# Optimization experiments

Measured on AMD Instinct MI355X. Metric: run time of the kernel, lower is better.

Reference implementation:

```python
import jax, jax.numpy as jnp
import numpy as np

N = 100000
E = 1600000
DIN = 128
HID = 128
EPS = 1e-5


def setup_inputs() -> dict:
    key = jax.random.key(0)
    ks = jax.random.split(key, 16)
    s = lambda i, shape, sc=0.05: jax.random.normal(ks[i], shape, dtype=jnp.float32) * sc
    inp = {
        "x": jax.random.normal(ks[0], (N, DIN), dtype=jnp.float32),
        "edge_index": jax.random.randint(ks[1], (2, E), 0, N, dtype=jnp.int64),
        # layer 1
        "W1": s(2, (DIN, HID)), "b1": jnp.zeros((HID,), jnp.float32),
        "g1": jnp.ones((HID,), jnp.float32), "be1": jnp.zeros((HID,), jnp.float32),
        "m1": s(3, (HID,)), "v1": jax.random.uniform(ks[4], (HID,), jnp.float32) + 0.5,
        # layer 2
        "W2": s(5, (HID, HID)), "b2": jnp.zeros((HID,), jnp.float32),
        "g2": jnp.ones((HID,), jnp.float32), "be2": jnp.zeros((HID,), jnp.float32),
        "m2": s(6, (HID,)), "v2": jax.random.uniform(ks[7], (HID,), jnp.float32) + 0.5,
        # classifier
        "Wc1": s(8, (HID, HID // 2)), "bc1": jnp.zeros((HID // 2,), jnp.float32),
        "Wc2": s(9, (HID // 2, 2)), "bc2": jnp.zeros((2,), jnp.float32),
    }
    return inp


def _gnn_layer(x, W, b, src, dst):
    # linear then scatter-mean of source features onto destinations
    h = x @ W + b                                    # [N, HID]
    msg_sum = jax.ops.segment_sum(h[src], dst, num_segments=N)   # [N, HID]
    cnt = jax.ops.segment_sum(jnp.ones((src.shape[0],), h.dtype), dst, num_segments=N)
    return msg_sum / cnt[:, None]                    # self-loops guarantee cnt >= 1


def _bn(x, g, be, m, v):
    return (x - m) * jax.lax.rsqrt(v + EPS) * g + be


def reference(x, edge_index, W1, b1, g1, be1, m1, v1, W2, b2, g2, be2, m2, v2, Wc1, bc1, Wc2, bc2):
    # add self loops (PyG add_self_loops appends [i, i])
    loop = jnp.arange(N, dtype=edge_index.dtype)
    src = jnp.concatenate([edge_index[0], loop])
    dst = jnp.concatenate([edge_index[1], loop])

    h = _gnn_layer(x, W1, b1, src, dst)
    h = jax.nn.relu(_bn(h, g1, be1, m1, v1))
    h = _gnn_layer(h, W2, b2, src, dst)
    h = jax.nn.relu(_bn(h, g2, be2, m2, v2))

    h = jax.nn.relu(h @ Wc1 + bc1)
    return h @ Wc2 + bc2                              # logits [N, 2]
```

## Files before the change

### kernel.cpp

```cpp
#include <hip/hip_runtime.h>
#include <hip/hip_bf16.h>

#define EPS 1e-5f

__global__ __launch_bounds__(256) void k_zero(int* p, int n) {
    int i = blockIdx.x * 256 + threadIdx.x;
    if (i < n) p[i] = 0;
}

__global__ __launch_bounds__(256) void k_hist(const int* __restrict__ dst,
                                              int* __restrict__ counts, int nE) {
    int i = blockIdx.x * 256 + threadIdx.x;
    if (i < nE) atomicAdd(&counts[dst[i]], 1);
}

__global__ __launch_bounds__(256) void k_scan1(const int* __restrict__ counts,
                                               int* __restrict__ bsums, int n) {
    __shared__ int sdata[256];
    int base = blockIdx.x * 2048;
    int t = threadIdx.x;
    int s = 0;
#pragma unroll
    for (int i = 0; i < 8; ++i) {
        int idx = base + t * 8 + i;
        if (idx < n) s += counts[idx];
    }
    sdata[t] = s;
    __syncthreads();
    for (int off = 128; off > 0; off >>= 1) {
        if (t < off) sdata[t] += sdata[t + off];
        __syncthreads();
    }
    if (t == 0) bsums[blockIdx.x] = sdata[0];
}

__global__ __launch_bounds__(64) void k_scan2(int* __restrict__ bsums, int nb) {
    if (threadIdx.x == 0 && blockIdx.x == 0) {
        int acc = 0;
        for (int i = 0; i < nb; ++i) { int v = bsums[i]; bsums[i] = acc; acc += v; }
    }
}

__global__ __launch_bounds__(256) void k_scan3(const int* __restrict__ counts,
                                               const int* __restrict__ bsums,
                                               int* __restrict__ rowstart,
                                               int n, int nE) {
    __shared__ int sth[256];
    int base = blockIdx.x * 2048;
    int t = threadIdx.x;
    int loc[8];
    int s = 0;
#pragma unroll
    for (int i = 0; i < 8; ++i) {
        int idx = base + t * 8 + i;
        loc[i] = s;
        s += (idx < n) ? counts[idx] : 0;
    }
    sth[t] = s;
    __syncthreads();
    for (int off = 1; off < 256; off <<= 1) {
        int tmp = (t >= off) ? sth[t - off] : 0;
        __syncthreads();
        sth[t] += tmp;
        __syncthreads();
    }
    int excl = sth[t] - s + bsums[blockIdx.x];
#pragma unroll
    for (int i = 0; i < 8; ++i) {
        int idx = base + t * 8 + i;
        if (idx < n) rowstart[idx] = excl + loc[i];
    }
    if (blockIdx.x == 0 && t == 0) rowstart[n] = nE;
}

__global__ __launch_bounds__(256) void k_fill(const int* __restrict__ srci,
                                              const int* __restrict__ dsti,
                                              int* __restrict__ cursor,
                                              int* __restrict__ col, int nE) {
    int e = blockIdx.x * 256 + threadIdx.x;
    if (e < nE) {
        int p = atomicAdd(&cursor[dsti[e]], 1);
        col[p] = srci[e];
    }
}

__global__ __launch_bounds__(256) void k_linear(const float* __restrict__ X,
                                                const float* __restrict__ W,
                                                const float* __restrict__ bias,
                                                float* __restrict__ out,
                                                int nRows) {
    __shared__ float xs[64][132];
    int row0 = blockIdx.x * 64;
    int tid = threadIdx.x;
    for (int i = tid; i < 64 * 32; i += 256) {
        int r = i >> 5, c4 = (i & 31) << 2;
        float4 v = make_float4(0.f, 0.f, 0.f, 0.f);
        int row = row0 + r;
        if (row < nRows) v = *(const float4*)(X + (size_t)row * 128 + c4);
        *(float4*)&xs[r][c4] = v;
    }
    __syncthreads();

    int cg = tid & 15, rg = tid >> 4;
    int c0 = cg * 8, r0 = rg * 4;
    float acc[4][8];
    float4 b0 = *(const float4*)(bias + c0);
    float4 b1 = *(const float4*)(bias + c0 + 4);
#pragma unroll
    for (int r = 0; r < 4; ++r) {
        acc[r][0] = b0.x; acc[r][1] = b0.y; acc[r][2] = b0.z; acc[r][3] = b0.w;
        acc[r][4] = b1.x; acc[r][5] = b1.y; acc[r][6] = b1.z; acc[r][7] = b1.w;
    }

    for (int k0 = 0; k0 < 128; k0 += 4) {
        float4 xv[4];
#pragma unroll
        for (int r = 0; r < 4; ++r) xv[r] = *(const float4*)&xs[r0 + r][k0];
#pragma unroll
        for (int kk = 0; kk < 4; ++kk) {
            int k = k0 + kk;
            float4 w0 = *(const float4*)(W + k * 128 + c0);
            float4 w1 = *(const float4*)(W + k * 128 + c0 + 4);
            float wv[8] = {w0.x, w0.y, w0.z, w0.w, w1.x, w1.y, w1.z, w1.w};
#pragma unroll
            for (int r = 0; r < 4; ++r) {
                float xk = (&xv[r].x)[kk];
#pragma unroll
                for (int j = 0; j < 8; ++j) acc[r][j] = fmaf(xk, wv[j], acc[r][j]);
            }
        }
    }

#pragma unroll
    for (int r = 0; r < 4; ++r) {
        int row = row0 + r0 + r;
        if (row >= nRows) continue;
        *(float4*)(out + (size_t)row * 128 + c0) =
            make_float4(acc[r][0], acc[r][1], acc[r][2], acc[r][3]);
        *(float4*)(out + (size_t)row * 128 + c0 + 4) =
            make_float4(acc[r][4], acc[r][5], acc[r][6], acc[r][7]);
    }
}

template <bool FUSE_BN>
__global__ __launch_bounds__(256) void k_gather(const float* __restrict__ src,
                                                const int* __restrict__ rowstart,
                                                const int* __restrict__ col,
                                                const float* __restrict__ g,
                                                const float* __restrict__ be,
                                                const float* __restrict__ m,
                                                const float* __restrict__ v,
                                                float* __restrict__ out, int nRows) {
    int r = blockIdx.x * 4 + (threadIdx.x >> 6);
    if (r >= nRows) return;
    int lane = threadIdx.x & 63;
    int d0 = lane * 2;
    int s = rowstart[r], e = rowstart[r + 1];

    float2 acc = *(const float2*)(src + (size_t)r * 128 + d0);
    int j = s;
    for (; j + 4 <= e; j += 4) {
        int c0i = col[j], c1i = col[j + 1], c2i = col[j + 2], c3i = col[j + 3];
        float2 a = *(const float2*)(src + (size_t)c0i * 128 + d0);
        float2 b = *(const float2*)(src + (size_t)c1i * 128 + d0);
        float2 c = *(const float2*)(src + (size_t)c2i * 128 + d0);
        float2 d = *(const float2*)(src + (size_t)c3i * 128 + d0);
        acc.x += (a.x + b.x) + (c.x + d.x);
        acc.y += (a.y + b.y) + (c.y + d.y);
    }
    for (; j < e; ++j) {
        int ci = col[j];
        float2 a = *(const float2*)(src + (size_t)ci * 128 + d0);
        acc.x += a.x;
        acc.y += a.y;
    }
    float rc = 1.0f / (float)(e - s + 1);
    float2 o;
    if (FUSE_BN) {
        float2 gv = *(const float2*)(g + d0);
        float2 bev = *(const float2*)(be + d0);
        float2 mv = *(const float2*)(m + d0);
        float2 vv = *(const float2*)(v + d0);
        o.x = fmaxf((acc.x * rc - mv.x) * rsqrtf(vv.x + EPS) * gv.x + bev.x, 0.f);
        o.y = fmaxf((acc.y * rc - mv.y) * rsqrtf(vv.y + EPS) * gv.y + bev.y, 0.f);
    } else {
        o.x = acc.x * rc;
        o.y = acc.y * rc;
    }
    *(float2*)(out + (size_t)r * 128 + d0) = o;
}

__global__ __launch_bounds__(256) void k_final(const float* __restrict__ xin,
                                               const float* __restrict__ Wc1,
                                               const float* __restrict__ bc1,
                                               const float* __restrict__ Wc2,
                                               const float* __restrict__ bc2,
                                               float* __restrict__ out, int nRows) {
    __shared__ float xs[32][132];
    __shared__ float w1s[128][64];
    __shared__ float hs[32][68];
    int row0 = blockIdx.x * 32;
    int tid = threadIdx.x;

    for (int i = tid; i < 2048; i += 256) {
        int kk = i >> 4, c4 = (i & 15) << 2;
        *(float4*)&w1s[kk][c4] = *(const float4*)(Wc1 + kk * 64 + c4);
    }
    for (int i = tid; i < 1024; i += 256) {
        int r = i >> 5, c4 = (i & 31) << 2;
        int row = row0 + r;
        float4 o = make_float4(0.f, 0.f, 0.f, 0.f);
        if (row < nRows) o = *(const float4*)(xin + (size_t)row * 128 + c4);
        *(float4*)&xs[r][c4] = o;
    }
    __syncthreads();

    int cg = tid & 15, rg = tid >> 4;
    int c0 = cg * 4, r0 = rg * 2;
    float acc[2][4];
    float4 bc = *(const float4*)(bc1 + c0);
    acc[0][0] = bc.x; acc[0][1] = bc.y; acc[0][2] = bc.z; acc[0][3] = bc.w;
    acc[1][0] = bc.x; acc[1][1] = bc.y; acc[1][2] = bc.z; acc[1][3] = bc.w;
    for (int k = 0; k < 128; ++k) {
        float4 w4 = *(const float4*)&w1s[k][c0];
        float x0 = xs[r0][k], x1 = xs[r0 + 1][k];
        acc[0][0] = fmaf(x0, w4.x, acc[0][0]);
        acc[0][1] = fmaf(x0, w4.y, acc[0][1]);
        acc[0][2] = fmaf(x0, w4.z, acc[0][2]);
        acc[0][3] = fmaf(x0, w4.w, acc[0][3]);
        acc[1][0] = fmaf(x1, w4.x, acc[1][0]);
        acc[1][1] = fmaf(x1, w4.y, acc[1][1]);
        acc[1][2] = fmaf(x1, w4.z, acc[1][2]);
        acc[1][3] = fmaf(x1, w4.w, acc[1][3]);
    }
    *(float4*)&hs[r0][c0] = make_float4(fmaxf(acc[0][0], 0.f), fmaxf(acc[0][1], 0.f),
                                        fmaxf(acc[0][2], 0.f), fmaxf(acc[0][3], 0.f));
    *(float4*)&hs[r0 + 1][c0] = make_float4(fmaxf(acc[1][0], 0.f), fmaxf(acc[1][1], 0.f),
                                            fmaxf(acc[1][2], 0.f), fmaxf(acc[1][3], 0.f));
    __syncthreads();

    if (tid < 64) {
        int r = tid >> 1, oc = tid & 1;
        float s = bc2[oc];
        for (int c = 0; c < 64; ++c) s = fmaf(hs[r][c], Wc2[c * 2 + oc], s);
        int row = row0 + r;
        if (row < nRows) out[(size_t)row * 2 + oc] = s;
    }
}

extern "C" void kernel_launch(void* const* d_in, const int* in_sizes, int n_in,
                              void* d_out, int out_size, void* d_ws, size_t ws_size,
                              hipStream_t stream) {
    const float* x   = (const float*)d_in[0];
    const int*   ei  = (const int*)d_in[1];
    const float* W1  = (const float*)d_in[2];
    const float* b1  = (const float*)d_in[3];
    const float* g1  = (const float*)d_in[4];
    const float* be1 = (const float*)d_in[5];
    const float* m1  = (const float*)d_in[6];
    const float* v1  = (const float*)d_in[7];
    const float* W2  = (const float*)d_in[8];
    const float* b2  = (const float*)d_in[9];
    const float* g2  = (const float*)d_in[10];
    const float* be2 = (const float*)d_in[11];
    const float* m2  = (const float*)d_in[12];
    const float* v2  = (const float*)d_in[13];
    const float* Wc1 = (const float*)d_in[14];
    const float* bc1 = (const float*)d_in[15];
    const float* Wc2 = (const float*)d_in[16];
    const float* bc2 = (const float*)d_in[17];

    const int N_ = in_sizes[0] / 128;
    const int E_ = in_sizes[1] / 2;
    const int* srci = ei;
    const int* dsti = ei + E_;

    float* A = (float*)d_ws;
    float* B = A + (size_t)N_ * 128;
    int* counts   = (int*)(B + (size_t)N_ * 128);
    int* rowstart = counts + N_;
    int* bsums    = rowstart + N_ + 1;
    int* col      = bsums + 256;

    const int nb = (N_ + 2047) / 2048;

    k_zero <<<(N_ + 255) / 256, 256, 0, stream>>>(counts, N_);
    k_hist <<<(E_ + 255) / 256, 256, 0, stream>>>(dsti, counts, E_);
    k_scan1<<<nb, 256, 0, stream>>>(counts, bsums, N_);
    k_scan2<<<1, 64, 0, stream>>>(bsums, nb);
    k_scan3<<<nb, 256, 0, stream>>>(counts, bsums, rowstart, N_, E_);
    hipMemcpyAsync(counts, rowstart, (size_t)N_ * sizeof(int),
                   hipMemcpyDeviceToDevice, stream);
    k_fill <<<(E_ + 255) / 256, 256, 0, stream>>>(srci, dsti, counts, col, E_);

    k_linear<<<(N_ + 63) / 64, 256, 0, stream>>>(x, W1, b1, A, N_);
    k_gather<true><<<(N_ + 3) / 4, 256, 0, stream>>>(A, rowstart, col,
                                                     g1, be1, m1, v1, B, N_);

    k_linear<<<(N_ + 63) / 64, 256, 0, stream>>>(B, W2, b2, A, N_);
    k_gather<true><<<(N_ + 3) / 4, 256, 0, stream>>>(A, rowstart, col,
                                                     g2, be2, m2, v2, B, N_);

    k_final<<<(N_ + 31) / 32, 256, 0, stream>>>(B, Wc1, bc1, Wc2, bc2,
                                                (float*)d_out, N_);
}
```

Baseline: 723.2 us.

## Two-pass bucketed CSR fill and widen gather unroll to eight

Builds the CSR column array in two passes. Edges are first partitioned into buckets of 64 destination nodes through a packed (dst,src) temp buffer, then scattered per destination from that bucket-ordered stream. This is meant to give the per-node atomics and col writes locality instead of random scatter across the whole array, at the cost of an extra pass over 8-byte temp entries. The gather loop also issues 8 independent row loads per iteration instead of 4 to increase memory-level parallelism. The temp buffer reuses workspace B before it is needed.

```diff
diff --git a/kernel.cpp b/kernel.cpp
--- a/kernel.cpp
+++ b/kernel.cpp
@@ -2,6 +2,7 @@
 #include <hip/hip_bf16.h>
 
 #define EPS 1e-5f
+#define BKSH 6
 
 __global__ __launch_bounds__(256) void k_zero(int* p, int n) {
     int i = blockIdx.x * 256 + threadIdx.x;
@@ -73,14 +74,35 @@
     if (blockIdx.x == 0 && t == 0) rowstart[n] = nE;
 }
 
-__global__ __launch_bounds__(256) void k_fill(const int* __restrict__ srci,
+__global__ __launch_bounds__(256) void k_binit(const int* __restrict__ rowstart,
+                                               int* __restrict__ bcursor, int nbk) {
+    int bk = blockIdx.x * 256 + threadIdx.x;
+    if (bk < nbk) bcursor[bk] = rowstart[bk << BKSH];
+}
+
+__global__ __launch_bounds__(256) void k_part(const int* __restrict__ srci,
                                               const int* __restrict__ dsti,
-                                              int* __restrict__ cursor,
-                                              int* __restrict__ col, int nE) {
+                                              int* __restrict__ bcursor,
+                                              unsigned long long* __restrict__ tmp,
+                                              int nE) {
     int e = blockIdx.x * 256 + threadIdx.x;
     if (e < nE) {
-        int p = atomicAdd(&cursor[dsti[e]], 1);
-        col[p] = srci[e];
+        int s = srci[e], d = dsti[e];
+        int p = atomicAdd(&bcursor[d >> BKSH], 1);
+        tmp[p] = ((unsigned long long)(unsigned)d << 32) | (unsigned)s;
+    }
+}
+
+__global__ __launch_bounds__(256) void k_fill2(const unsigned long long* __restrict__ tmp,
+                                               int* __restrict__ cursor,
+                                               int* __restrict__ col, int nE) {
+    int e = blockIdx.x * 256 + threadIdx.x;
+    if (e < nE) {
+        unsigned long long v = tmp[e];
+        int d = (int)(v >> 32);
+        int s = (int)(v & 0xffffffffu);
+        int q = atomicAdd(&cursor[d], 1);
+        col[q] = s;
     }
 }
 
@@ -159,14 +181,16 @@
 
     float2 acc = *(const float2*)(src + (size_t)r * 128 + d0);
     int j = s;
-    for (; j + 4 <= e; j += 4) {
-        int c0i = col[j], c1i = col[j + 1], c2i = col[j + 2], c3i = col[j + 3];
-        float2 a = *(const float2*)(src + (size_t)c0i * 128 + d0);
-        float2 b = *(const float2*)(src + (size_t)c1i * 128 + d0);
-        float2 c = *(const float2*)(src + (size_t)c2i * 128 + d0);
-        float2 d = *(const float2*)(src + (size_t)c3i * 128 + d0);
-        acc.x += (a.x + b.x) + (c.x + d.x);
-        acc.y += (a.y + b.y) + (c.y + d.y);
+    for (; j + 8 <= e; j += 8) {
+        int ci[8];
+#pragma unroll
+        for (int u = 0; u < 8; ++u) ci[u] = col[j + u];
+        float2 t[8];
+#pragma unroll
+        for (int u = 0; u < 8; ++u)
+            t[u] = *(const float2*)(src + (size_t)ci[u] * 128 + d0);
+#pragma unroll
+        for (int u = 0; u < 8; ++u) { acc.x += t[u].x; acc.y += t[u].y; }
     }
     for (; j < e; ++j) {
         int ci = col[j];
@@ -274,13 +298,16 @@
     const int E_ = in_sizes[1] / 2;
     const int* srci = ei;
     const int* dsti = ei + E_;
+    const int NBK = (N_ + 63) >> BKSH;
 
     float* A = (float*)d_ws;
     float* B = A + (size_t)N_ * 128;
+    unsigned long long* tmp = (unsigned long long*)B;
     int* counts   = (int*)(B + (size_t)N_ * 128);
     int* rowstart = counts + N_;
     int* bsums    = rowstart + N_ + 1;
-    int* col      = bsums + 256;
+    int* bcursor  = bsums + 256;
+    int* col      = bcursor + 2048;
 
     const int nb = (N_ + 2047) / 2048;
 
@@ -289,9 +316,11 @@
     k_scan1<<<nb, 256, 0, stream>>>(counts, bsums, N_);
     k_scan2<<<1, 64, 0, stream>>>(bsums, nb);
     k_scan3<<<nb, 256, 0, stream>>>(counts, bsums, rowstart, N_, E_);
+    k_binit<<<(NBK + 255) / 256, 256, 0, stream>>>(rowstart, bcursor, NBK);
+    k_part <<<(E_ + 255) / 256, 256, 0, stream>>>(srci, dsti, bcursor, tmp, E_);
     hipMemcpyAsync(counts, rowstart, (size_t)N_ * sizeof(int),
                    hipMemcpyDeviceToDevice, stream);
-    k_fill <<<(E_ + 255) / 256, 256, 0, stream>>>(srci, dsti, counts, col, E_);
+    k_fill2<<<(E_ + 255) / 256, 256, 0, stream>>>(tmp, counts, col, E_);
 
     k_linear<<<(N_ + 63) / 64, 256, 0, stream>>>(x, W1, b1, A, N_);
     k_gather<true><<<(N_ + 3) / 4, 256, 0, stream>>>(A, rowstart, col,
```

Result: slower. 899.1 us (+24.3%).
